# Optimization experiments

Measured on AMD Instinct MI355X. Metric: run time of the kernel, lower is better.

Reference implementation:

```python
import jax, jax.numpy as jnp
import numpy as np

B, L, HID, NH = 4, 1024, 768, 12
D = HID // NH  # 64 per-head
SCALE = 1.0 / np.sqrt(D).astype(np.float32)
NEG = -1e15


def layer_norm(x, g, b, eps=1e-5):
    m = x.mean(-1, keepdims=True)
    v = ((x - m) ** 2).mean(-1, keepdims=True)
    return (x - m) / jnp.sqrt(v + eps) * g + b


def setup_inputs() -> dict:
    key = jax.random.key(0)
    ks = jax.random.split(key, 20)
    s = 0.02
    inp = jax.random.normal(ks[0], (B, L, HID), jnp.float32)
    seq_len = jax.random.randint(ks[1], (B,), 1, L + 1).astype(jnp.int32)
    rel_pos_embedding = jax.random.normal(ks[2], (B, NH, L, L), jnp.float32)
    def lin(k):
        k1, k2 = jax.random.split(k)
        W = jax.random.normal(k1, (HID, HID), jnp.float32) * s  # stored [in,out]
        b = jax.random.normal(k2, (HID,), jnp.float32) * s
        return W, b
    Wq, bq = lin(ks[3])
    Wk, bk = lin(ks[4])
    Wv, bv = lin(ks[5])
    Wo, bo = lin(ks[6])  # attn ff_final
    W0, b0 = lin(ks[7])  # FFN layer 0 (ff_size == hidden_size)
    W1, b1 = lin(ks[8])  # FFN layer 1
    ln_g = jnp.ones((HID,), jnp.float32)
    ln_b = jnp.zeros((HID,), jnp.float32)
    return {"inp": inp, "seq_len": seq_len, "lex_num": 0,
            "rel_pos_embedding": rel_pos_embedding,
            "Wq": Wq, "bq": bq, "Wk": Wk, "bk": bk, "Wv": Wv, "bv": bv,
            "Wo": Wo, "bo": bo, "W0": W0, "b0": b0, "W1": W1, "b1": b1,
            "ln_g": ln_g, "ln_b": ln_b}


def reference(inp, seq_len, lex_num, rel_pos_embedding,
              Wq, bq, Wk, bk, Wv, bv, Wo, bo, W0, b0, W1, b1, ln_g, ln_b):
    # layer_preprocess: '' -> identity
    x = inp
    # --- attention (q=k=v=x) ---
    q = (x @ Wq + bq).reshape(B, L, NH, D)
    k = (x @ Wk + bk).reshape(B, L, NH, D)
    v = (x @ Wv + bv).reshape(B, L, NH, D)
    scores = jnp.einsum('blhd,bmhd->bhlm', q, k) * SCALE + rel_pos_embedding
    valid = jnp.arange(L)[None, :] < (seq_len + lex_num)[:, None]  # [B,L]
    scores = jnp.where(valid[:, None, None, :], scores, NEG)
    attn = jax.nn.softmax(scores, axis=-1)  # attn dropout: eval mode -> identity
    ctx = jnp.einsum('bhlm,bmhd->blhd', attn, v).reshape(B, L, HID)
    y = ctx @ Wo + bo  # ff_final
    # layer_postprocess 'an': output = output + inp(of process); then LayerNorm
    y = layer_norm(y + y, ln_g, ln_b)
    # layer_preprocess '' -> identity, then FFN [hid, hid, hid]
    h = y @ W0 + b0
    h = jax.nn.relu(h)
    h = h @ W1 + b1
    out = layer_norm(h + h, ln_g, ln_b)
    return out
```

## Files before the change

### kernel.cpp

```cpp
#include <hip/hip_runtime.h>
#include <math.h>

#define B_   4
#define L_   1024
#define HID_ 768
#define NH_  12
#define D_   64
#define SCALE_ 0.125f
#define NEGV (-1e15f)

typedef __attribute__((ext_vector_type(4))) float  f32x4;
typedef __attribute__((ext_vector_type(8))) __bf16 bf16x8;
typedef __attribute__((ext_vector_type(8))) unsigned short ushort8v;
typedef __attribute__((ext_vector_type(4))) unsigned short ushort4v;

typedef const __attribute__((address_space(1))) unsigned int* gas1_t;
typedef __attribute__((address_space(3))) unsigned int*       las3_t;
#define GLDS16(g, l) __builtin_amdgcn_global_load_lds((gas1_t)(g), (las3_t)(l), 16, 0, 0)

static __device__ __forceinline__ unsigned short f2bf(float f) {
    unsigned int u = __builtin_bit_cast(unsigned int, f);
    u += 0x7fffu + ((u >> 16) & 1u);
    return (unsigned short)(u >> 16);
}

__global__ __launch_bounds__(256) void convert_x_kernel(
    const float* __restrict__ in, unsigned short* __restrict__ out, int n4)
{
    int i = blockIdx.x * 256 + threadIdx.x;
    if (i < n4) {
        float4 v = reinterpret_cast<const float4*>(in)[i];
        ushort4v o;
        o.x = f2bf(v.x); o.y = f2bf(v.y); o.z = f2bf(v.z); o.w = f2bf(v.w);
        reinterpret_cast<ushort4v*>(out)[i] = o;
    }
}

struct WArgs { const float* w[6]; unsigned short* wt[6]; };

__global__ __launch_bounds__(256) void transpose_w_kernel(WArgs a)
{
    const float* W = a.w[blockIdx.z];
    unsigned short* Wt = a.wt[blockIdx.z];
    __shared__ float t[64][65];
    const int tid = threadIdx.x;
    const int lr = tid >> 2, lc4 = (tid & 3) * 16;
    const int r0 = blockIdx.y * 64, c0 = blockIdx.x * 64;
#pragma unroll
    for (int j = 0; j < 4; ++j) {
        float4 v = *reinterpret_cast<const float4*>(&W[(size_t)(r0 + lr) * HID_ + c0 + lc4 + j * 4]);
        t[lr][lc4 + j * 4 + 0] = v.x;
        t[lr][lc4 + j * 4 + 1] = v.y;
        t[lr][lc4 + j * 4 + 2] = v.z;
        t[lr][lc4 + j * 4 + 3] = v.w;
    }
    __syncthreads();
    unsigned short tmp[16];
#pragma unroll
    for (int j = 0; j < 16; ++j) tmp[j] = f2bf(t[lc4 + j][lr]);
    unsigned short* dst = &Wt[(size_t)(c0 + lr) * HID_ + r0 + lc4];
    *reinterpret_cast<ushort8v*>(dst)     = *reinterpret_cast<ushort8v*>(&tmp[0]);
    *reinterpret_cast<ushort8v*>(dst + 8) = *reinterpret_cast<ushort8v*>(&tmp[8]);
}

struct GemmJob {
    const unsigned short* A;
    const unsigned short* Wt;
    const float* bias;
    void* C;
    int mode;
    int relu;
    float scale;
};
struct GemmArgs { GemmJob j[3]; };

__global__ __launch_bounds__(256, 4) void gemm_bf16_kernel(GemmArgs args)
{
    const GemmJob jb = args.j[blockIdx.z];
    __shared__ unsigned short As[64 * 64];
    __shared__ unsigned short Bs[128 * 64];

    const int tid = threadIdx.x;
    const int w = tid >> 6, lane = tid & 63, g = lane >> 4, lq = lane & 15;
    const int m0 = blockIdx.x * 64, n0 = blockIdx.y * 128;

    f32x4 acc[4][2];
#pragma unroll
    for (int i = 0; i < 4; ++i)
#pragma unroll
        for (int j = 0; j < 2; ++j) acc[i][j] = (f32x4){0.f, 0.f, 0.f, 0.f};

    const int sr = tid >> 3;
    const int kq = ((tid & 7) ^ (sr & 7)) * 8;
    const unsigned short* Ap0 = jb.A  + (size_t)(m0 + sr) * HID_ + kq;
    const unsigned short* Ap1 = jb.A  + (size_t)(m0 + 32 + sr) * HID_ + kq;
    const unsigned short* Bp0 = jb.Wt + (size_t)(n0 + sr) * HID_ + kq;
    const unsigned short* Bp1 = jb.Wt + (size_t)(n0 + 32 + sr) * HID_ + kq;
    const unsigned short* Bp2 = jb.Wt + (size_t)(n0 + 64 + sr) * HID_ + kq;
    const unsigned short* Bp3 = jb.Wt + (size_t)(n0 + 96 + sr) * HID_ + kq;
    char* AsB = (char*)As;
    char* BsB = (char*)Bs;
    const int wb = w * 1024;

    for (int k0 = 0; k0 < HID_; k0 += 64) {
        __syncthreads();
        GLDS16(Ap0 + k0, AsB + wb);
        GLDS16(Ap1 + k0, AsB + 4096 + wb);
        GLDS16(Bp0 + k0, BsB + wb);
        GLDS16(Bp1 + k0, BsB + 4096 + wb);
        GLDS16(Bp2 + k0, BsB + 8192 + wb);
        GLDS16(Bp3 + k0, BsB + 12288 + wb);
        __syncthreads();

#pragma unroll
        for (int ks = 0; ks < 2; ++ks) {
            bf16x8 af[4], bf[2];
#pragma unroll
            for (int mi = 0; mi < 4; ++mi) {
                int row = mi * 16 + lq;
                int c = (ks * 4 + g) ^ (row & 7);
                af[mi] = *reinterpret_cast<const bf16x8*>(&As[row * 64 + c * 8]);
            }
#pragma unroll
            for (int ni = 0; ni < 2; ++ni) {
                int row = w * 32 + ni * 16 + lq;
                int c = (ks * 4 + g) ^ (row & 7);
                bf[ni] = *reinterpret_cast<const bf16x8*>(&Bs[row * 64 + c * 8]);
            }
            __builtin_amdgcn_s_setprio(1);
#pragma unroll
            for (int mi = 0; mi < 4; ++mi)
#pragma unroll
                for (int ni = 0; ni < 2; ++ni)
                    acc[mi][ni] = __builtin_amdgcn_mfma_f32_16x16x32_bf16(
                        af[mi], bf[ni], acc[mi][ni], 0, 0, 0);
            __builtin_amdgcn_s_setprio(0);
        }
    }

    float bcol[2];
#pragma unroll
    for (int ni = 0; ni < 2; ++ni) bcol[ni] = jb.bias[n0 + w * 32 + ni * 16 + lq];

#pragma unroll
    for (int mi = 0; mi < 4; ++mi) {
#pragma unroll
        for (int ni = 0; ni < 2; ++ni) {
            const int n = n0 + w * 32 + ni * 16 + lq;
            float v[4];
#pragma unroll
            for (int r = 0; r < 4; ++r) {
                float x = (acc[mi][ni][r] + bcol[ni]) * jb.scale;
                if (jb.relu) x = fmaxf(x, 0.f);
                v[r] = x;
            }
            const int mbase = m0 + mi * 16 + 4 * g;
            if (jb.mode == 0) {
                float* C = (float*)jb.C;
#pragma unroll
                for (int r = 0; r < 4; ++r)
                    C[(size_t)(mbase + r) * HID_ + n] = v[r];
            } else if (jb.mode == 1) {
                unsigned short* C = (unsigned short*)jb.C;
#pragma unroll
                for (int r = 0; r < 4; ++r)
                    C[(size_t)(mbase + r) * HID_ + n] = f2bf(v[r]);
            } else {
                unsigned short* C = (unsigned short*)jb.C;
                const int bb = mbase >> 10, ltok = mbase & 1023;
                ushort4v o;
                o.x = f2bf(v[0]); o.y = f2bf(v[1]); o.z = f2bf(v[2]); o.w = f2bf(v[3]);
                *reinterpret_cast<ushort4v*>(&C[(size_t)(bb * HID_ + n) * L_ + ltok]) = o;
            }
        }
    }
}

__global__ __launch_bounds__(256, 3) void attn_mfma_kernel(
    const unsigned short* __restrict__ Qb, const unsigned short* __restrict__ Kb,
    const unsigned short* __restrict__ Vtb, const float* __restrict__ rel,
    const int* __restrict__ seq_len, const int* __restrict__ lex_num,
    unsigned short* __restrict__ ctx)
{
    const int qt = blockIdx.x, bh = blockIdx.y;
    const int b = bh / NH_, h = bh % NH_;
    const int q0 = qt * 64;
    const int sl = seq_len[b] + lex_num[0];
    const int nkt = (sl + 127) >> 7;

    __shared__ unsigned short Ks[128 * 64];
    __shared__ unsigned short Vs[64 * 128];
    __shared__ unsigned short Ps[64 * 136];

    const int tid = threadIdx.x;
    const int w = tid >> 6, lane = tid & 63, g = lane >> 4, lq = lane & 15;

    const int rK = tid >> 3, cK = (tid & 7) * 8;
    const int rV = tid >> 4, cV = (tid & 15) * 8;
    const unsigned short* Kbase = Kb  + (size_t)(b * L_) * HID_ + h * D_;
    const unsigned short* Vbase = Vtb + (size_t)(b * HID_ + h * D_) * L_;
    char* KsB = (char*)Ks;
    char* VsB = (char*)Vs;
    const int wb = w * 1024;

    const float* relbase = rel + (size_t)bh * (L_ * L_) + (size_t)(q0 + w * 16 + 4 * g) * L_ + lq;

    bf16x8 aq[2];
#pragma unroll
    for (int ks = 0; ks < 2; ++ks)
        aq[ks] = *reinterpret_cast<const bf16x8*>(
            &Qb[(size_t)(b * L_ + q0 + w * 16 + lq) * HID_ + h * D_ + ks * 32 + g * 8]);

    f32x4 acc[4];
    float m_r[4], l_r[4];
#pragma unroll
    for (int i = 0; i < 4; ++i) {
        acc[i] = (f32x4){0.f, 0.f, 0.f, 0.f};
        m_r[i] = -3e38f; l_r[i] = 0.f;
    }

    for (int kt = 0; kt < nkt; ++kt) {
        const int k0 = kt * 128;
        __syncthreads();

#pragma unroll
        for (int j = 0; j < 4; ++j)
            GLDS16(&Kbase[(size_t)(k0 + j * 32 + rK) * HID_ + cK], KsB + j * 4096 + wb);
#pragma unroll
        for (int j = 0; j < 4; ++j)
            GLDS16(&Vbase[(size_t)(j * 16 + rV) * L_ + k0 + cV], VsB + j * 4096 + wb);

        float rv[8][4];
#pragma unroll
        for (int ni = 0; ni < 8; ++ni)
#pragma unroll
            for (int r = 0; r < 4; ++r)
                rv[ni][r] = relbase[(size_t)r * L_ + k0 + ni * 16];

        __syncthreads();

        f32x4 s[8];
#pragma unroll
        for (int ni = 0; ni < 8; ++ni) s[ni] = (f32x4){0.f, 0.f, 0.f, 0.f};
        __builtin_amdgcn_s_setprio(1);
#pragma unroll
        for (int ks = 0; ks < 2; ++ks)
#pragma unroll
            for (int ni = 0; ni < 8; ++ni) {
                bf16x8 bk = *reinterpret_cast<const bf16x8*>(
                    &Ks[(ni * 16 + lq) * 64 + ks * 32 + g * 8]);
                s[ni] = __builtin_amdgcn_mfma_f32_16x16x32_bf16(aq[ks], bk, s[ni], 0, 0, 0);
            }
        __builtin_amdgcn_s_setprio(0);

        float sv[8][4];
#pragma unroll
        for (int ni = 0; ni < 8; ++ni) {
            const int col = k0 + ni * 16 + lq;
            const bool ok = col < sl;
#pragma unroll
            for (int r = 0; r < 4; ++r)
                sv[ni][r] = ok ? (s[ni][r] + rv[ni][r]) : NEGV;
        }

#pragma unroll
        for (int r = 0; r < 4; ++r) {
            float rm = sv[0][r];
#pragma unroll
            for (int ni = 1; ni < 8; ++ni) rm = fmaxf(rm, sv[ni][r]);
            rm = fmaxf(rm, __shfl_xor(rm, 1, 16));
            rm = fmaxf(rm, __shfl_xor(rm, 2, 16));
            rm = fmaxf(rm, __shfl_xor(rm, 4, 16));
            rm = fmaxf(rm, __shfl_xor(rm, 8, 16));
            float mn = fmaxf(m_r[r], rm);
            float sc = __expf(m_r[r] - mn);
            float p[8], rs = 0.f;
#pragma unroll
            for (int ni = 0; ni < 8; ++ni) {
                p[ni] = __expf(sv[ni][r] - mn);
                rs += p[ni];
            }
            rs += __shfl_xor(rs, 1, 16);
            rs += __shfl_xor(rs, 2, 16);
            rs += __shfl_xor(rs, 4, 16);
            rs += __shfl_xor(rs, 8, 16);
            l_r[r] = l_r[r] * sc + rs;
            m_r[r] = mn;
#pragma unroll
            for (int ni = 0; ni < 4; ++ni) acc[ni][r] *= sc;
#pragma unroll
            for (int ni = 0; ni < 8; ++ni)
                Ps[(w * 16 + 4 * g + r) * 136 + ni * 16 + lq] = f2bf(p[ni]);
        }

        __builtin_amdgcn_s_setprio(1);
#pragma unroll
        for (int ks = 0; ks < 4; ++ks) {
            bf16x8 ap = *reinterpret_cast<const bf16x8*>(
                &Ps[(w * 16 + lq) * 136 + ks * 32 + g * 8]);
#pragma unroll
            for (int ni = 0; ni < 4; ++ni) {
                bf16x8 bv = *reinterpret_cast<const bf16x8*>(
                    &Vs[(ni * 16 + lq) * 128 + ks * 32 + g * 8]);
                acc[ni] = __builtin_amdgcn_mfma_f32_16x16x32_bf16(ap, bv, acc[ni], 0, 0, 0);
            }
        }
        __builtin_amdgcn_s_setprio(0);
    }

    float inv[4];
#pragma unroll
    for (int r = 0; r < 4; ++r) inv[r] = 1.f / l_r[r];
#pragma unroll
    for (int ni = 0; ni < 4; ++ni)
#pragma unroll
        for (int r = 0; r < 4; ++r)
            ctx[(size_t)(b * L_ + q0 + w * 16 + 4 * g + r) * HID_ + h * D_ + ni * 16 + lq] =
                f2bf(acc[ni][r] * inv[r]);
}

__global__ __launch_bounds__(256) void ln2_kernel(
    const float* __restrict__ in, const float* __restrict__ g,
    const float* __restrict__ bta, void* __restrict__ out, int bf16out)
{
    const int row = blockIdx.x;
    const float* x = in + (size_t)row * HID_;
    const int tid = threadIdx.x;

    float vals[3];
    float s = 0.f, ss = 0.f;
#pragma unroll
    for (int j = 0; j < 3; ++j) {
        float t = 2.f * x[tid + j * 256];
        vals[j] = t;
        s += t;
        ss += t * t;
    }
#pragma unroll
    for (int m = 1; m < 64; m <<= 1) {
        s += __shfl_xor(s, m, 64);
        ss += __shfl_xor(ss, m, 64);
    }
    __shared__ float sb[4], ssb[4];
    if ((tid & 63) == 0) { sb[tid >> 6] = s; ssb[tid >> 6] = ss; }
    __syncthreads();
    s = sb[0] + sb[1] + sb[2] + sb[3];
    ss = ssb[0] + ssb[1] + ssb[2] + ssb[3];
    const float mean = s * (1.f / 768.f);
    float var = ss * (1.f / 768.f) - mean * mean;
    if (var < 0.f) var = 0.f;
    const float invs = rsqrtf(var + 1e-5f);
    if (bf16out) {
        unsigned short* o = (unsigned short*)out;
#pragma unroll
        for (int j = 0; j < 3; ++j) {
            int c = tid + j * 256;
            o[(size_t)row * HID_ + c] = f2bf((vals[j] - mean) * invs * g[c] + bta[c]);
        }
    } else {
        float* o = (float*)out;
#pragma unroll
        for (int j = 0; j < 3; ++j) {
            int c = tid + j * 256;
            o[(size_t)row * HID_ + c] = (vals[j] - mean) * invs * g[c] + bta[c];
        }
    }
}

extern "C" void kernel_launch(void* const* d_in, const int* in_sizes, int n_in,
                              void* d_out, int out_size, void* d_ws, size_t ws_size,
                              hipStream_t stream) {
    const float* inp     = (const float*)d_in[0];
    const int*   seq_len = (const int*)d_in[1];
    const int*   lex_num = (const int*)d_in[2];
    const float* rel     = (const float*)d_in[3];
    const float* Wq = (const float*)d_in[4];
    const float* bq = (const float*)d_in[5];
    const float* Wk = (const float*)d_in[6];
    const float* bk = (const float*)d_in[7];
    const float* Wv = (const float*)d_in[8];
    const float* bv = (const float*)d_in[9];
    const float* Wo = (const float*)d_in[10];
    const float* bo = (const float*)d_in[11];
    const float* W0 = (const float*)d_in[12];
    const float* b0 = (const float*)d_in[13];
    const float* W1 = (const float*)d_in[14];
    const float* b1 = (const float*)d_in[15];
    const float* ln_g = (const float*)d_in[16];
    const float* ln_b = (const float*)d_in[17];
    float* out = (float*)d_out;

    char* W = (char*)d_ws;
    const size_t WT_SZ = (size_t)HID_ * HID_ * 2;
    unsigned short* Wt[6];
    for (int i = 0; i < 6; ++i) Wt[i] = (unsigned short*)(W + i * WT_SZ);
    size_t off = 6 * WT_SZ;
    const size_t TOK_BF = (size_t)B_ * L_ * HID_ * 2;
    unsigned short* qb  = (unsigned short*)(W + off); off += TOK_BF;
    unsigned short* kb  = (unsigned short*)(W + off); off += TOK_BF;
    unsigned short* vtb = (unsigned short*)(W + off); off += TOK_BF;
    unsigned short* Eb  = (unsigned short*)(W + off); off += TOK_BF;
    float* Fbuf = (float*)(W + off);

    unsigned short* Xb   = Eb;
    unsigned short* ctxb = Eb;
    unsigned short* y2b  = vtb;
    unsigned short* hb   = qb;

    convert_x_kernel<<<dim3(3072), dim3(256), 0, stream>>>(inp, Xb, (B_ * L_ * HID_) / 4);

    {
        WArgs wa;
        const float* ws_[6] = {Wq, Wk, Wv, Wo, W0, W1};
        for (int i = 0; i < 6; ++i) { wa.w[i] = ws_[i]; wa.wt[i] = Wt[i]; }
        transpose_w_kernel<<<dim3(12, 12, 6), dim3(256), 0, stream>>>(wa);
    }

    {
        GemmArgs ga;
        ga.j[0] = {Xb, Wt[0], bq, (void*)qb,  1, 0, SCALE_};
        ga.j[1] = {Xb, Wt[1], bk, (void*)kb,  1, 0, 1.f};
        ga.j[2] = {Xb, Wt[2], bv, (void*)vtb, 2, 0, 1.f};
        gemm_bf16_kernel<<<dim3(64, 6, 3), dim3(256), 0, stream>>>(ga);
    }

    attn_mfma_kernel<<<dim3(16, 48), dim3(256), 0, stream>>>(
        qb, kb, vtb, rel, seq_len, lex_num, ctxb);

    {
        GemmArgs ga;
        ga.j[0] = {ctxb, Wt[3], bo, (void*)Fbuf, 0, 0, 1.f};
        gemm_bf16_kernel<<<dim3(64, 6, 1), dim3(256), 0, stream>>>(ga);
    }
    ln2_kernel<<<dim3(4096), dim3(256), 0, stream>>>(Fbuf, ln_g, ln_b, (void*)y2b, 1);
    {
        GemmArgs ga;
        ga.j[0] = {y2b, Wt[4], b0, (void*)hb, 1, 1, 1.f};
        gemm_bf16_kernel<<<dim3(64, 6, 1), dim3(256), 0, stream>>>(ga);
    }
    {
        GemmArgs ga;
        ga.j[0] = {hb, Wt[5], b1, (void*)Fbuf, 0, 0, 1.f};
        gemm_bf16_kernel<<<dim3(64, 6, 1), dim3(256), 0, stream>>>(ga);
    }
    ln2_kernel<<<dim3(4096), dim3(256), 0, stream>>>(Fbuf, ln_g, ln_b, (void*)out, 0);
}
```

Measured before the change: 142.3 us.

## Restructure attention into single-wave blocks loading K/V directly to registers

Each attention block becomes one 64-thread wave handling a 16-query strip, with 64-key tiles loaded straight from global memory into registers. The shared K/V staging and the __syncthreads barriers are removed, and the grid grows from 16x48 to 64x48 blocks. The aim is to cut barrier stalls and raise occupancy and scheduling flexibility. The cost is that K/V are no longer shared across four waves, so global and L2 traffic for K/V rises about fourfold, and the rel_pos loads stay the dominant stream.

Result: slower. 166.9 us (+17.3%).

```diff
diff --git a/kernel.cpp b/kernel.cpp
--- a/kernel.cpp
+++ b/kernel.cpp
@@ -176,40 +176,32 @@
     }
 }
 
-__global__ __launch_bounds__(256, 3) void attn_mfma_kernel(
+__global__ __launch_bounds__(64) void attn_mfma_kernel(
     const unsigned short* __restrict__ Qb, const unsigned short* __restrict__ Kb,
     const unsigned short* __restrict__ Vtb, const float* __restrict__ rel,
     const int* __restrict__ seq_len, const int* __restrict__ lex_num,
     unsigned short* __restrict__ ctx)
 {
-    const int qt = blockIdx.x, bh = blockIdx.y;
+    const int strip = blockIdx.x, bh = blockIdx.y;
     const int b = bh / NH_, h = bh % NH_;
-    const int q0 = qt * 64;
+    const int q0 = strip * 16;
     const int sl = seq_len[b] + lex_num[0];
-    const int nkt = (sl + 127) >> 7;
-
-    __shared__ unsigned short Ks[128 * 64];
-    __shared__ unsigned short Vs[64 * 128];
-    __shared__ unsigned short Ps[64 * 136];
-
-    const int tid = threadIdx.x;
-    const int w = tid >> 6, lane = tid & 63, g = lane >> 4, lq = lane & 15;
-
-    const int rK = tid >> 3, cK = (tid & 7) * 8;
-    const int rV = tid >> 4, cV = (tid & 15) * 8;
+    const int nkt = (sl + 63) >> 6;
+
+    __shared__ unsigned short Ps[16 * 72];
+
+    const int lane = threadIdx.x;
+    const int g = lane >> 4, lq = lane & 15;
+
     const unsigned short* Kbase = Kb  + (size_t)(b * L_) * HID_ + h * D_;
     const unsigned short* Vbase = Vtb + (size_t)(b * HID_ + h * D_) * L_;
-    char* KsB = (char*)Ks;
-    char* VsB = (char*)Vs;
-    const int wb = w * 1024;
-
-    const float* relbase = rel + (size_t)bh * (L_ * L_) + (size_t)(q0 + w * 16 + 4 * g) * L_ + lq;
+    const float* relbase = rel + (size_t)bh * (L_ * L_) + (size_t)(q0 + 4 * g) * L_ + lq;
 
     bf16x8 aq[2];
 #pragma unroll
     for (int ks = 0; ks < 2; ++ks)
         aq[ks] = *reinterpret_cast<const bf16x8*>(
-            &Qb[(size_t)(b * L_ + q0 + w * 16 + lq) * HID_ + h * D_ + ks * 32 + g * 8]);
+            &Qb[(size_t)(b * L_ + q0 + lq) * HID_ + h * D_ + ks * 32 + g * 8]);
 
     f32x4 acc[4];
     float m_r[4], l_r[4];
@@ -220,63 +212,59 @@
     }
 
     for (int kt = 0; kt < nkt; ++kt) {
-        const int k0 = kt * 128;
-        __syncthreads();
-
-#pragma unroll
-        for (int j = 0; j < 4; ++j)
-            GLDS16(&Kbase[(size_t)(k0 + j * 32 + rK) * HID_ + cK], KsB + j * 4096 + wb);
-#pragma unroll
-        for (int j = 0; j < 4; ++j)
-            GLDS16(&Vbase[(size_t)(j * 16 + rV) * L_ + k0 + cV], VsB + j * 4096 + wb);
-
-        float rv[8][4];
-#pragma unroll
-        for (int ni = 0; ni < 8; ++ni)
+        const int k0 = kt * 64;
+
+        bf16x8 bk[2][4], bv[2][4];
+#pragma unroll
+        for (int ks = 0; ks < 2; ++ks)
+#pragma unroll
+            for (int ni = 0; ni < 4; ++ni) {
+                bk[ks][ni] = *reinterpret_cast<const bf16x8*>(
+                    &Kbase[(size_t)(k0 + ni * 16 + lq) * HID_ + ks * 32 + g * 8]);
+                bv[ks][ni] = *reinterpret_cast<const bf16x8*>(
+                    &Vbase[(size_t)(ni * 16 + lq) * L_ + k0 + ks * 32 + g * 8]);
+            }
+        float rv[16];
+#pragma unroll
+        for (int ni = 0; ni < 4; ++ni)
 #pragma unroll
             for (int r = 0; r < 4; ++r)
-                rv[ni][r] = relbase[(size_t)r * L_ + k0 + ni * 16];
-
-        __syncthreads();
-
-        f32x4 s[8];
-#pragma unroll
-        for (int ni = 0; ni < 8; ++ni) s[ni] = (f32x4){0.f, 0.f, 0.f, 0.f};
+                rv[ni * 4 + r] = relbase[(size_t)r * L_ + k0 + ni * 16];
+
+        f32x4 s[4];
+#pragma unroll
+        for (int ni = 0; ni < 4; ++ni) s[ni] = (f32x4){0.f, 0.f, 0.f, 0.f};
         __builtin_amdgcn_s_setprio(1);
 #pragma unroll
         for (int ks = 0; ks < 2; ++ks)
 #pragma unroll
-            for (int ni = 0; ni < 8; ++ni) {
-                bf16x8 bk = *reinterpret_cast<const bf16x8*>(
-                    &Ks[(ni * 16 + lq) * 64 + ks * 32 + g * 8]);
-                s[ni] = __builtin_amdgcn_mfma_f32_16x16x32_bf16(aq[ks], bk, s[ni], 0, 0, 0);
-            }
+            for (int ni = 0; ni < 4; ++ni)
+                s[ni] = __builtin_amdgcn_mfma_f32_16x16x32_bf16(
+                    aq[ks], bk[ks][ni], s[ni], 0, 0, 0);
         __builtin_amdgcn_s_setprio(0);
 
-        float sv[8][4];
-#pragma unroll
-        for (int ni = 0; ni < 8; ++ni) {
+        float sv[4][4];
+#pragma unroll
+        for (int ni = 0; ni < 4; ++ni) {
             const int col = k0 + ni * 16 + lq;
             const bool ok = col < sl;
 #pragma unroll
             for (int r = 0; r < 4; ++r)
-                sv[ni][r] = ok ? (s[ni][r] + rv[ni][r]) : NEGV;
+                sv[ni][r] = ok ? (s[ni][r] + rv[ni * 4 + r]) : NEGV;
         }
 
 #pragma unroll
         for (int r = 0; r < 4; ++r) {
-            float rm = sv[0][r];
-#pragma unroll
-            for (int ni = 1; ni < 8; ++ni) rm = fmaxf(rm, sv[ni][r]);
+            float rm = fmaxf(fmaxf(sv[0][r], sv[1][r]), fmaxf(sv[2][r], sv[3][r]));
             rm = fmaxf(rm, __shfl_xor(rm, 1, 16));
             rm = fmaxf(rm, __shfl_xor(rm, 2, 16));
             rm = fmaxf(rm, __shfl_xor(rm, 4, 16));
             rm = fmaxf(rm, __shfl_xor(rm, 8, 16));
             float mn = fmaxf(m_r[r], rm);
             float sc = __expf(m_r[r] - mn);
-            float p[8], rs = 0.f;
-#pragma unroll
-            for (int ni = 0; ni < 8; ++ni) {
+            float p[4], rs = 0.f;
+#pragma unroll
+            for (int ni = 0; ni < 4; ++ni) {
                 p[ni] = __expf(sv[ni][r] - mn);
                 rs += p[ni];
             }
@@ -287,23 +275,21 @@
             l_r[r] = l_r[r] * sc + rs;
             m_r[r] = mn;
 #pragma unroll
-            for (int ni = 0; ni < 4; ++ni) acc[ni][r] *= sc;
-#pragma unroll
-            for (int ni = 0; ni < 8; ++ni)
-                Ps[(w * 16 + 4 * g + r) * 136 + ni * 16 + lq] = f2bf(p[ni]);
+            for (int ni = 0; ni < 4; ++ni) {
+                acc[ni][r] *= sc;
+                Ps[(4 * g + r) * 72 + ni * 16 + lq] = f2bf(p[ni]);
+            }
         }
 
         __builtin_amdgcn_s_setprio(1);
 #pragma unroll
-        for (int ks = 0; ks < 4; ++ks) {
+        for (int ks = 0; ks < 2; ++ks) {
             bf16x8 ap = *reinterpret_cast<const bf16x8*>(
-                &Ps[(w * 16 + lq) * 136 + ks * 32 + g * 8]);
-#pragma unroll
-            for (int ni = 0; ni < 4; ++ni) {
-                bf16x8 bv = *reinterpret_cast<const bf16x8*>(
-                    &Vs[(ni * 16 + lq) * 128 + ks * 32 + g * 8]);
-                acc[ni] = __builtin_amdgcn_mfma_f32_16x16x32_bf16(ap, bv, acc[ni], 0, 0, 0);
-            }
+                &Ps[lq * 72 + ks * 32 + g * 8]);
+#pragma unroll
+            for (int ni = 0; ni < 4; ++ni)
+                acc[ni] = __builtin_amdgcn_mfma_f32_16x16x32_bf16(
+                    ap, bv[ks][ni], acc[ni], 0, 0, 0);
         }
         __builtin_amdgcn_s_setprio(0);
     }
@@ -315,7 +301,7 @@
     for (int ni = 0; ni < 4; ++ni)
 #pragma unroll
         for (int r = 0; r < 4; ++r)
-            ctx[(size_t)(b * L_ + q0 + w * 16 + 4 * g + r) * HID_ + h * D_ + ni * 16 + lq] =
+            ctx[(size_t)(b * L_ + q0 + 4 * g + r) * HID_ + h * D_ + ni * 16 + lq] =
                 f2bf(acc[ni][r] * inv[r]);
 }
 
@@ -424,7 +410,7 @@
         gemm_bf16_kernel<<<dim3(64, 6, 3), dim3(256), 0, stream>>>(ga);
     }
 
-    attn_mfma_kernel<<<dim3(16, 48), dim3(256), 0, stream>>>(
+    attn_mfma_kernel<<<dim3(64, 48), dim3(64), 0, stream>>>(
         qb, kb, vtb, rel, seq_len, lex_num, ctxb);
 
     {
```
